# Optimization experiments

Measured on AMD Instinct MI355X. Metric: run time of the kernel, lower is better.

Reference implementation:

```python
import jax, jax.numpy as jnp
import numpy as np

NEG_SLOPE = 0.2

def setup_inputs() -> dict:
    key = jax.random.key(0)
    ks = jax.random.split(key, 6)
    N, C, H, E_DIM, E = 50000, 128, 64, 16, 800000
    x = jax.random.normal(ks[0], (N, C), dtype=jnp.float32)
    edge_index = jax.random.randint(ks[1], (2, E), 0, N, dtype=jnp.int64)
    edge_attr = jax.random.normal(ks[2], (E, E_DIM), dtype=jnp.float32)
    fc_w = jax.random.normal(ks[3], (H, C), dtype=jnp.float32) * (1.0 / np.sqrt(C))
    fc_b = jnp.zeros((H,), dtype=jnp.float32)
    att_w = jax.random.normal(ks[4], (H, 2 * H + E_DIM), dtype=jnp.float32) * (1.0 / np.sqrt(2 * H + E_DIM))
    att_b = jnp.zeros((H,), dtype=jnp.float32)
    return {"x": x, "edge_index": edge_index, "edge_attr": edge_attr,
            "fc_w": fc_w, "fc_b": fc_b, "att_w": att_w, "att_b": att_b}

def reference(x, edge_index, edge_attr, fc_w, fc_b, att_w, att_b):
    # Node projection: h = fc(x), [N, H]
    h = x @ fc_w.T + fc_b
    src = edge_index[0]  # i (destination of aggregation)
    dst = edge_index[1]  # j (neighbor whose features are aggregated)
    h_i = h[src]                      # [E, H]
    h_j = h[dst]                      # [E, H]
    feat = jnp.concatenate([h_i, h_j, edge_attr], axis=-1)  # [E, 2H+edge_dim]
    alpha = jax.nn.leaky_relu(feat @ att_w.T + att_b, negative_slope=NEG_SLOPE)  # [E, H]
    # dropout is identity in eval mode (training=False)
    msg = h_j * alpha                 # [E, H]
    out = jax.ops.segment_sum(msg, src, num_segments=h.shape[0])  # scatter-add into out[i]
    return out
```

## Files before the change

kernel.cpp:

```cpp
#include <hip/hip_runtime.h>


#define HID 64

__global__ __launch_bounds__(256) void node_kernel(
    const float* __restrict__ x,
    const float* __restrict__ fc_w, const float* __restrict__ fc_b,
    const float* __restrict__ att_w, const float* __restrict__ att_b,
    float* __restrict__ ai_out, float2* __restrict__ hjaj_out, int N)
{
    __shared__ __align__(16) float4 wF[64 * 32];
    __shared__ __align__(16) float4 wI[64 * 16];
    __shared__ __align__(16) float4 wJ[64 * 16];
    __shared__ __align__(16) float xs[4][128];
    __shared__ __align__(16) float hs[4][64];

    const int t = threadIdx.x;
    for (int idx = t; idx < 64 * 32; idx += 256) {
        int l = idx >> 5, c = idx & 31;
        wF[l * 32 + (c ^ (l & 31))] =
            *reinterpret_cast<const float4*>(fc_w + l * 128 + c * 4);
    }
    for (int idx = t; idx < 64 * 16; idx += 256) {
        int l = idx >> 4, c = idx & 15;
        wI[l * 16 + (c ^ (l & 15))] =
            *reinterpret_cast<const float4*>(att_w + l * 144 + c * 4);
        wJ[l * 16 + (c ^ (l & 15))] =
            *reinterpret_cast<const float4*>(att_w + l * 144 + 64 + c * 4);
    }
    __syncthreads();

    const int w = t >> 6, l = t & 63;
    const float bF = fc_b[l];
    const float bA = att_b[l];
    const int waveId = blockIdx.x * 4 + w;
    const int nWaves = gridDim.x * 4;

    for (int n = waveId; n < N; n += nWaves) {
        float2 xv = reinterpret_cast<const float2*>(x)[n * 64 + l];
        xs[w][2 * l] = xv.x;
        xs[w][2 * l + 1] = xv.y;
        float acc = bF;
        #pragma unroll
        for (int c = 0; c < 32; ++c) {
            float4 wv = wF[l * 32 + (c ^ (l & 31))];
            float4 xc = *reinterpret_cast<const float4*>(&xs[w][c * 4]);
            acc = fmaf(wv.x, xc.x, acc);
            acc = fmaf(wv.y, xc.y, acc);
            acc = fmaf(wv.z, xc.z, acc);
            acc = fmaf(wv.w, xc.w, acc);
        }
        hs[w][l] = acc;
        float a2 = bA, a3 = 0.f;
        #pragma unroll
        for (int c = 0; c < 16; ++c) {
            float4 hv = *reinterpret_cast<const float4*>(&hs[w][c * 4]);
            float4 wi = wI[l * 16 + (c ^ (l & 15))];
            float4 wj = wJ[l * 16 + (c ^ (l & 15))];
            a2 = fmaf(wi.x, hv.x, a2); a2 = fmaf(wi.y, hv.y, a2);
            a2 = fmaf(wi.z, hv.z, a2); a2 = fmaf(wi.w, hv.w, a2);
            a3 = fmaf(wj.x, hv.x, a3); a3 = fmaf(wj.y, hv.y, a3);
            a3 = fmaf(wj.z, hv.z, a3); a3 = fmaf(wj.w, hv.w, a3);
        }
        ai_out[n * 64 + l] = a2;
        hjaj_out[n * 64 + l] = make_float2(acc, a3);
    }
}

__global__ __launch_bounds__(256) void edge_kernel(
    const int* __restrict__ ei,
    const float* __restrict__ ea,
    const float* __restrict__ ai,
    const float2* __restrict__ hjaj,
    const float* __restrict__ att_w,
    float* __restrict__ out, int E)
{
    __shared__ __align__(16) float4 eas[4][256];

    const int t = threadIdx.x;
    const int w = t >> 6, l = t & 63;

    float we[16];
    #pragma unroll
    for (int k = 0; k < 16; ++k) we[k] = att_w[l * 144 + 128 + k];

    const int waveId = blockIdx.x * 4 + w;
    const int nWaves = gridDim.x * 4;
    const float4* ea4 = reinterpret_cast<const float4*>(ea);

    for (int e0 = waveId * 64; e0 < E; e0 += nWaves * 64) {
        const int nE = min(64, E - e0);
        int src = 0, dst = 0;
        if (l < nE) {
            src = ei[e0 + l];
            dst = ei[E + e0 + l];
        }
        #pragma unroll
        for (int r = 0; r < 4; ++r) {
            int f = r * 64 + l;
            if (f < nE * 4) eas[w][f] = ea4[(size_t)e0 * 4 + f];
        }
        asm volatile("s_waitcnt lgkmcnt(0)" ::: "memory");

        for (int e = 0; e < nE; ++e) {
            int s = __shfl(src, e);
            int d = __shfl(dst, e);
            float a_src = ai[s * 64 + l];
            float2 hd = hjaj[d * 64 + l];
            float4 v0 = eas[w][e * 4 + 0];
            float4 v1 = eas[w][e * 4 + 1];
            float4 v2 = eas[w][e * 4 + 2];
            float4 v3 = eas[w][e * 4 + 3];
            float pre = a_src + hd.y;
            pre = fmaf(we[0], v0.x, pre);  pre = fmaf(we[1], v0.y, pre);
            pre = fmaf(we[2], v0.z, pre);  pre = fmaf(we[3], v0.w, pre);
            pre = fmaf(we[4], v1.x, pre);  pre = fmaf(we[5], v1.y, pre);
            pre = fmaf(we[6], v1.z, pre);  pre = fmaf(we[7], v1.w, pre);
            pre = fmaf(we[8], v2.x, pre);  pre = fmaf(we[9], v2.y, pre);
            pre = fmaf(we[10], v2.z, pre); pre = fmaf(we[11], v2.w, pre);
            pre = fmaf(we[12], v3.x, pre); pre = fmaf(we[13], v3.y, pre);
            pre = fmaf(we[14], v3.z, pre); pre = fmaf(we[15], v3.w, pre);
            float alpha = pre > 0.f ? pre : 0.2f * pre;
            atomicAdd(&out[(size_t)s * 64 + l], hd.x * alpha);
        }
    }
}

extern "C" void kernel_launch(void* const* d_in, const int* in_sizes, int n_in,
                              void* d_out, int out_size, void* d_ws, size_t ws_size,
                              hipStream_t stream) {
    const float* x     = (const float*)d_in[0];
    const int*   ei    = (const int*)d_in[1];
    const float* ea    = (const float*)d_in[2];
    const float* fc_w  = (const float*)d_in[3];
    const float* fc_b  = (const float*)d_in[4];
    const float* att_w = (const float*)d_in[5];
    const float* att_b = (const float*)d_in[6];
    float* out = (float*)d_out;

    const int N = in_sizes[0] / 128;
    const int E = in_sizes[2] / 16;

    float*  ai   = (float*)d_ws;
    float2* hjaj = (float2*)((char*)d_ws + (size_t)N * 64 * sizeof(float));

    hipMemsetAsync(d_out, 0, (size_t)out_size * sizeof(float), stream);

    node_kernel<<<512, 256, 0, stream>>>(x, fc_w, fc_b, att_w, att_b, ai, hjaj, N);
    edge_kernel<<<1024, 256, 0, stream>>>(ei, ea, ai, hjaj, att_w, out, E);
}
```

Baseline: 284.0 us.

## Batch four edges per gather group and four nodes per wave in projection

Measured after the change: 266.8 us. 1.06x faster.

```diff
diff --git a/kernel.cpp b/kernel.cpp
--- a/kernel.cpp
+++ b/kernel.cpp
@@ -1,7 +1,5 @@
 #include <hip/hip_runtime.h>
 
-
-#define HID 64
 
 __global__ __launch_bounds__(256) void node_kernel(
     const float* __restrict__ x,
@@ -12,8 +10,8 @@
     __shared__ __align__(16) float4 wF[64 * 32];
     __shared__ __align__(16) float4 wI[64 * 16];
     __shared__ __align__(16) float4 wJ[64 * 16];
-    __shared__ __align__(16) float xs[4][128];
-    __shared__ __align__(16) float hs[4][64];
+    __shared__ __align__(16) float xs[4][4][128];
+    __shared__ __align__(16) float hs[4][4][64];
 
     const int t = threadIdx.x;
     for (int idx = t; idx < 64 * 32; idx += 256) {
@@ -35,35 +33,55 @@
     const float bA = att_b[l];
     const int waveId = blockIdx.x * 4 + w;
     const int nWaves = gridDim.x * 4;
-
-    for (int n = waveId; n < N; n += nWaves) {
-        float2 xv = reinterpret_cast<const float2*>(x)[n * 64 + l];
-        xs[w][2 * l] = xv.x;
-        xs[w][2 * l + 1] = xv.y;
-        float acc = bF;
+    const float2* x2 = reinterpret_cast<const float2*>(x);
+
+    for (int n0 = waveId * 4; n0 < N; n0 += nWaves * 4) {
+        const int nb = min(4, N - n0);
+        #pragma unroll
+        for (int m = 0; m < 4; ++m) {
+            if (m < nb) {
+                float2 xv = x2[(size_t)(n0 + m) * 64 + l];
+                xs[w][m][2 * l] = xv.x;
+                xs[w][m][2 * l + 1] = xv.y;
+            }
+        }
+        float acc[4] = {bF, bF, bF, bF};
         #pragma unroll
         for (int c = 0; c < 32; ++c) {
             float4 wv = wF[l * 32 + (c ^ (l & 31))];
-            float4 xc = *reinterpret_cast<const float4*>(&xs[w][c * 4]);
-            acc = fmaf(wv.x, xc.x, acc);
-            acc = fmaf(wv.y, xc.y, acc);
-            acc = fmaf(wv.z, xc.z, acc);
-            acc = fmaf(wv.w, xc.w, acc);
-        }
-        hs[w][l] = acc;
-        float a2 = bA, a3 = 0.f;
+            #pragma unroll
+            for (int m = 0; m < 4; ++m) {
+                float4 xc = *reinterpret_cast<const float4*>(&xs[w][m][c * 4]);
+                acc[m] = fmaf(wv.x, xc.x, acc[m]);
+                acc[m] = fmaf(wv.y, xc.y, acc[m]);
+                acc[m] = fmaf(wv.z, xc.z, acc[m]);
+                acc[m] = fmaf(wv.w, xc.w, acc[m]);
+            }
+        }
+        #pragma unroll
+        for (int m = 0; m < 4; ++m) hs[w][m][l] = acc[m];
+        float a2[4] = {bA, bA, bA, bA};
+        float a3[4] = {0.f, 0.f, 0.f, 0.f};
         #pragma unroll
         for (int c = 0; c < 16; ++c) {
-            float4 hv = *reinterpret_cast<const float4*>(&hs[w][c * 4]);
             float4 wi = wI[l * 16 + (c ^ (l & 15))];
             float4 wj = wJ[l * 16 + (c ^ (l & 15))];
-            a2 = fmaf(wi.x, hv.x, a2); a2 = fmaf(wi.y, hv.y, a2);
-            a2 = fmaf(wi.z, hv.z, a2); a2 = fmaf(wi.w, hv.w, a2);
-            a3 = fmaf(wj.x, hv.x, a3); a3 = fmaf(wj.y, hv.y, a3);
-            a3 = fmaf(wj.z, hv.z, a3); a3 = fmaf(wj.w, hv.w, a3);
-        }
-        ai_out[n * 64 + l] = a2;
-        hjaj_out[n * 64 + l] = make_float2(acc, a3);
+            #pragma unroll
+            for (int m = 0; m < 4; ++m) {
+                float4 hv = *reinterpret_cast<const float4*>(&hs[w][m][c * 4]);
+                a2[m] = fmaf(wi.x, hv.x, a2[m]); a2[m] = fmaf(wi.y, hv.y, a2[m]);
+                a2[m] = fmaf(wi.z, hv.z, a2[m]); a2[m] = fmaf(wi.w, hv.w, a2[m]);
+                a3[m] = fmaf(wj.x, hv.x, a3[m]); a3[m] = fmaf(wj.y, hv.y, a3[m]);
+                a3[m] = fmaf(wj.z, hv.z, a3[m]); a3[m] = fmaf(wj.w, hv.w, a3[m]);
+            }
+        }
+        #pragma unroll
+        for (int m = 0; m < 4; ++m) {
+            if (m < nb) {
+                ai_out[(size_t)(n0 + m) * 64 + l] = a2[m];
+                hjaj_out[(size_t)(n0 + m) * 64 + l] = make_float2(acc[m], a3[m]);
+            }
+        }
     }
 }
 
@@ -87,43 +105,75 @@
     const int waveId = blockIdx.x * 4 + w;
     const int nWaves = gridDim.x * 4;
     const float4* ea4 = reinterpret_cast<const float4*>(ea);
-
-    for (int e0 = waveId * 64; e0 < E; e0 += nWaves * 64) {
-        const int nE = min(64, E - e0);
+    const int fullE = E & ~63;
+
+#define EDGE_COMPUTE(S, HD, IDX)                                               \
+    {                                                                          \
+        float4 v0 = eas[w][(IDX) * 4 + 0];                                     \
+        float4 v1 = eas[w][(IDX) * 4 + 1];                                     \
+        float4 v2 = eas[w][(IDX) * 4 + 2];                                     \
+        float4 v3 = eas[w][(IDX) * 4 + 3];                                     \
+        float pre = (HD).y + a_##S;                                            \
+        pre = fmaf(we[0], v0.x, pre);  pre = fmaf(we[1], v0.y, pre);           \
+        pre = fmaf(we[2], v0.z, pre);  pre = fmaf(we[3], v0.w, pre);           \
+        pre = fmaf(we[4], v1.x, pre);  pre = fmaf(we[5], v1.y, pre);           \
+        pre = fmaf(we[6], v1.z, pre);  pre = fmaf(we[7], v1.w, pre);           \
+        pre = fmaf(we[8], v2.x, pre);  pre = fmaf(we[9], v2.y, pre);           \
+        pre = fmaf(we[10], v2.z, pre); pre = fmaf(we[11], v2.w, pre);          \
+        pre = fmaf(we[12], v3.x, pre); pre = fmaf(we[13], v3.y, pre);          \
+        pre = fmaf(we[14], v3.z, pre); pre = fmaf(we[15], v3.w, pre);          \
+        float alpha = pre > 0.f ? pre : 0.2f * pre;                            \
+        atomicAdd(&out[(size_t)s_##S * 64 + l], (HD).x * alpha);               \
+    }
+
+    for (int e0 = waveId * 64; e0 < fullE; e0 += nWaves * 64) {
+        int src = ei[e0 + l];
+        int dst = ei[E + e0 + l];
+        #pragma unroll
+        for (int r = 0; r < 4; ++r)
+            eas[w][r * 64 + l] = ea4[(size_t)e0 * 4 + r * 64 + l];
+        asm volatile("s_waitcnt lgkmcnt(0)" ::: "memory");
+
+        #pragma unroll 1
+        for (int g = 0; g < 64; g += 4) {
+            int s_0 = __shfl(src, g + 0), s_1 = __shfl(src, g + 1);
+            int s_2 = __shfl(src, g + 2), s_3 = __shfl(src, g + 3);
+            int d_0 = __shfl(dst, g + 0), d_1 = __shfl(dst, g + 1);
+            int d_2 = __shfl(dst, g + 2), d_3 = __shfl(dst, g + 3);
+            float a_0 = ai[(size_t)s_0 * 64 + l];
+            float a_1 = ai[(size_t)s_1 * 64 + l];
+            float a_2 = ai[(size_t)s_2 * 64 + l];
+            float a_3 = ai[(size_t)s_3 * 64 + l];
+            float2 h0 = hjaj[(size_t)d_0 * 64 + l];
+            float2 h1 = hjaj[(size_t)d_1 * 64 + l];
+            float2 h2 = hjaj[(size_t)d_2 * 64 + l];
+            float2 h3 = hjaj[(size_t)d_3 * 64 + l];
+            EDGE_COMPUTE(0, h0, g + 0);
+            EDGE_COMPUTE(1, h1, g + 1);
+            EDGE_COMPUTE(2, h2, g + 2);
+            EDGE_COMPUTE(3, h3, g + 3);
+        }
+    }
+
+    if (E > fullE && waveId == 0) {
+        const int nE = E - fullE;
         int src = 0, dst = 0;
-        if (l < nE) {
-            src = ei[e0 + l];
-            dst = ei[E + e0 + l];
-        }
+        if (l < nE) { src = ei[fullE + l]; dst = ei[E + fullE + l]; }
         #pragma unroll
         for (int r = 0; r < 4; ++r) {
             int f = r * 64 + l;
-            if (f < nE * 4) eas[w][f] = ea4[(size_t)e0 * 4 + f];
+            if (f < nE * 4) eas[w][f] = ea4[(size_t)fullE * 4 + f];
         }
         asm volatile("s_waitcnt lgkmcnt(0)" ::: "memory");
-
         for (int e = 0; e < nE; ++e) {
-            int s = __shfl(src, e);
-            int d = __shfl(dst, e);
-            float a_src = ai[s * 64 + l];
-            float2 hd = hjaj[d * 64 + l];
-            float4 v0 = eas[w][e * 4 + 0];
-            float4 v1 = eas[w][e * 4 + 1];
-            float4 v2 = eas[w][e * 4 + 2];
-            float4 v3 = eas[w][e * 4 + 3];
-            float pre = a_src + hd.y;
-            pre = fmaf(we[0], v0.x, pre);  pre = fmaf(we[1], v0.y, pre);
-            pre = fmaf(we[2], v0.z, pre);  pre = fmaf(we[3], v0.w, pre);
-            pre = fmaf(we[4], v1.x, pre);  pre = fmaf(we[5], v1.y, pre);
-            pre = fmaf(we[6], v1.z, pre);  pre = fmaf(we[7], v1.w, pre);
-            pre = fmaf(we[8], v2.x, pre);  pre = fmaf(we[9], v2.y, pre);
-            pre = fmaf(we[10], v2.z, pre); pre = fmaf(we[11], v2.w, pre);
-            pre = fmaf(we[12], v3.x, pre); pre = fmaf(we[13], v3.y, pre);
-            pre = fmaf(we[14], v3.z, pre); pre = fmaf(we[15], v3.w, pre);
-            float alpha = pre > 0.f ? pre : 0.2f * pre;
-            atomicAdd(&out[(size_t)s * 64 + l], hd.x * alpha);
-        }
-    }
+            int s_0 = __shfl(src, e);
+            int d_0 = __shfl(dst, e);
+            float a_0 = ai[(size_t)s_0 * 64 + l];
+            float2 h0 = hjaj[(size_t)d_0 * 64 + l];
+            EDGE_COMPUTE(0, h0, e);
+        }
+    }
+#undef EDGE_COMPUTE
 }
 
 extern "C" void kernel_launch(void* const* d_in, const int* in_sizes, int n_in,
@@ -147,5 +197,5 @@
     hipMemsetAsync(d_out, 0, (size_t)out_size * sizeof(float), stream);
 
     node_kernel<<<512, 256, 0, stream>>>(x, fc_w, fc_b, att_w, att_b, ai, hjaj, N);
-    edge_kernel<<<1024, 256, 0, stream>>>(ei, ea, ai, hjaj, att_w, out, E);
+    edge_kernel<<<2048, 256, 0, stream>>>(ei, ea, ai, hjaj, att_w, out, E);
 }
```

## Software-pipeline edge gathers, one tile per wave, and batch two nodes per wave

Applied to the files above, without the earlier changes.

After: 450.9 us. 58.8% more time.

```diff
diff --git a/kernel.cpp b/kernel.cpp
--- a/kernel.cpp
+++ b/kernel.cpp
@@ -1,9 +1,7 @@
 #include <hip/hip_runtime.h>
 
 
-#define HID 64
-
-__global__ __launch_bounds__(256) void node_kernel(
+__global__ __launch_bounds__(512) void node_kernel(
     const float* __restrict__ x,
     const float* __restrict__ fc_w, const float* __restrict__ fc_b,
     const float* __restrict__ att_w, const float* __restrict__ att_b,
@@ -12,16 +10,16 @@
     __shared__ __align__(16) float4 wF[64 * 32];
     __shared__ __align__(16) float4 wI[64 * 16];
     __shared__ __align__(16) float4 wJ[64 * 16];
-    __shared__ __align__(16) float xs[4][128];
-    __shared__ __align__(16) float hs[4][64];
+    __shared__ __align__(16) float xs[8][2][128];
+    __shared__ __align__(16) float hs[8][2][64];
 
     const int t = threadIdx.x;
-    for (int idx = t; idx < 64 * 32; idx += 256) {
+    for (int idx = t; idx < 64 * 32; idx += 512) {
         int l = idx >> 5, c = idx & 31;
         wF[l * 32 + (c ^ (l & 31))] =
             *reinterpret_cast<const float4*>(fc_w + l * 128 + c * 4);
     }
-    for (int idx = t; idx < 64 * 16; idx += 256) {
+    for (int idx = t; idx < 64 * 16; idx += 512) {
         int l = idx >> 4, c = idx & 15;
         wI[l * 16 + (c ^ (l & 15))] =
             *reinterpret_cast<const float4*>(att_w + l * 144 + c * 4);
@@ -33,37 +31,57 @@
     const int w = t >> 6, l = t & 63;
     const float bF = fc_b[l];
     const float bA = att_b[l];
-    const int waveId = blockIdx.x * 4 + w;
-    const int nWaves = gridDim.x * 4;
-
-    for (int n = waveId; n < N; n += nWaves) {
-        float2 xv = reinterpret_cast<const float2*>(x)[n * 64 + l];
-        xs[w][2 * l] = xv.x;
-        xs[w][2 * l + 1] = xv.y;
-        float acc = bF;
+    const int waveId = blockIdx.x * 8 + w;
+    const int nWaves = gridDim.x * 8;
+    const float2* x2 = reinterpret_cast<const float2*>(x);
+
+    for (int n0 = waveId * 2; n0 < N; n0 += nWaves * 2) {
+        const int nb = min(2, N - n0);
+        #pragma unroll
+        for (int m = 0; m < 2; ++m) {
+            if (m < nb) {
+                float2 xv = x2[(size_t)(n0 + m) * 64 + l];
+                xs[w][m][2 * l] = xv.x;
+                xs[w][m][2 * l + 1] = xv.y;
+            }
+        }
+        float acc[2] = {bF, bF};
         #pragma unroll
         for (int c = 0; c < 32; ++c) {
             float4 wv = wF[l * 32 + (c ^ (l & 31))];
-            float4 xc = *reinterpret_cast<const float4*>(&xs[w][c * 4]);
-            acc = fmaf(wv.x, xc.x, acc);
-            acc = fmaf(wv.y, xc.y, acc);
-            acc = fmaf(wv.z, xc.z, acc);
-            acc = fmaf(wv.w, xc.w, acc);
-        }
-        hs[w][l] = acc;
-        float a2 = bA, a3 = 0.f;
+            #pragma unroll
+            for (int m = 0; m < 2; ++m) {
+                float4 xc = *reinterpret_cast<const float4*>(&xs[w][m][c * 4]);
+                acc[m] = fmaf(wv.x, xc.x, acc[m]);
+                acc[m] = fmaf(wv.y, xc.y, acc[m]);
+                acc[m] = fmaf(wv.z, xc.z, acc[m]);
+                acc[m] = fmaf(wv.w, xc.w, acc[m]);
+            }
+        }
+        #pragma unroll
+        for (int m = 0; m < 2; ++m) hs[w][m][l] = acc[m];
+        float a2[2] = {bA, bA};
+        float a3[2] = {0.f, 0.f};
         #pragma unroll
         for (int c = 0; c < 16; ++c) {
-            float4 hv = *reinterpret_cast<const float4*>(&hs[w][c * 4]);
             float4 wi = wI[l * 16 + (c ^ (l & 15))];
             float4 wj = wJ[l * 16 + (c ^ (l & 15))];
-            a2 = fmaf(wi.x, hv.x, a2); a2 = fmaf(wi.y, hv.y, a2);
-            a2 = fmaf(wi.z, hv.z, a2); a2 = fmaf(wi.w, hv.w, a2);
-            a3 = fmaf(wj.x, hv.x, a3); a3 = fmaf(wj.y, hv.y, a3);
-            a3 = fmaf(wj.z, hv.z, a3); a3 = fmaf(wj.w, hv.w, a3);
-        }
-        ai_out[n * 64 + l] = a2;
-        hjaj_out[n * 64 + l] = make_float2(acc, a3);
+            #pragma unroll
+            for (int m = 0; m < 2; ++m) {
+                float4 hv = *reinterpret_cast<const float4*>(&hs[w][m][c * 4]);
+                a2[m] = fmaf(wi.x, hv.x, a2[m]); a2[m] = fmaf(wi.y, hv.y, a2[m]);
+                a2[m] = fmaf(wi.z, hv.z, a2[m]); a2[m] = fmaf(wi.w, hv.w, a2[m]);
+                a3[m] = fmaf(wj.x, hv.x, a3[m]); a3[m] = fmaf(wj.y, hv.y, a3[m]);
+                a3[m] = fmaf(wj.z, hv.z, a3[m]); a3[m] = fmaf(wj.w, hv.w, a3[m]);
+            }
+        }
+        #pragma unroll
+        for (int m = 0; m < 2; ++m) {
+            if (m < nb) {
+                ai_out[(size_t)(n0 + m) * 64 + l] = a2[m];
+                hjaj_out[(size_t)(n0 + m) * 64 + l] = make_float2(acc[m], a3[m]);
+            }
+        }
     }
 }
 
@@ -85,33 +103,77 @@
     for (int k = 0; k < 16; ++k) we[k] = att_w[l * 144 + 128 + k];
 
     const int waveId = blockIdx.x * 4 + w;
-    const int nWaves = gridDim.x * 4;
+    const int e0 = waveId * 64;
+    if (e0 >= E) return;
+    const int nE = min(64, E - e0);
+
+    int src = 0, dst = 0;
+    if (l < nE) { src = ei[e0 + l]; dst = ei[E + e0 + l]; }
     const float4* ea4 = reinterpret_cast<const float4*>(ea);
-
-    for (int e0 = waveId * 64; e0 < E; e0 += nWaves * 64) {
-        const int nE = min(64, E - e0);
-        int src = 0, dst = 0;
-        if (l < nE) {
-            src = ei[e0 + l];
-            dst = ei[E + e0 + l];
-        }
-        #pragma unroll
-        for (int r = 0; r < 4; ++r) {
-            int f = r * 64 + l;
-            if (f < nE * 4) eas[w][f] = ea4[(size_t)e0 * 4 + f];
-        }
-        asm volatile("s_waitcnt lgkmcnt(0)" ::: "memory");
-
+    #pragma unroll
+    for (int r = 0; r < 4; ++r) {
+        int f = r * 64 + l;
+        if (f < nE * 4) eas[w][f] = ea4[(size_t)e0 * 4 + f];
+    }
+    asm volatile("s_waitcnt lgkmcnt(0)" ::: "memory");
+
+#define LOADG(S, g)                                                            \
+    {                                                                          \
+        _Pragma("unroll") for (int e = 0; e < 4; ++e) {                        \
+            s##S[e] = __shfl(src, (g) * 4 + e);                                \
+            int dd = __shfl(dst, (g) * 4 + e);                                 \
+            a##S[e] = ai[(size_t)s##S[e] * 64 + l];                            \
+            h##S[e] = hjaj[(size_t)dd * 64 + l];                               \
+        }                                                                      \
+    }
+
+#define COMPG(S, g)                                                            \
+    {                                                                          \
+        _Pragma("unroll") for (int e = 0; e < 4; ++e) {                        \
+            float4 v0 = eas[w][((g) * 4 + e) * 4 + 0];                         \
+            float4 v1 = eas[w][((g) * 4 + e) * 4 + 1];                         \
+            float4 v2 = eas[w][((g) * 4 + e) * 4 + 2];                         \
+            float4 v3 = eas[w][((g) * 4 + e) * 4 + 3];                         \
+            float pre = h##S[e].y + a##S[e];                                   \
+            pre = fmaf(we[0], v0.x, pre);  pre = fmaf(we[1], v0.y, pre);       \
+            pre = fmaf(we[2], v0.z, pre);  pre = fmaf(we[3], v0.w, pre);       \
+            pre = fmaf(we[4], v1.x, pre);  pre = fmaf(we[5], v1.y, pre);       \
+            pre = fmaf(we[6], v1.z, pre);  pre = fmaf(we[7], v1.w, pre);       \
+            pre = fmaf(we[8], v2.x, pre);  pre = fmaf(we[9], v2.y, pre);       \
+            pre = fmaf(we[10], v2.z, pre); pre = fmaf(we[11], v2.w, pre);      \
+            pre = fmaf(we[12], v3.x, pre); pre = fmaf(we[13], v3.y, pre);      \
+            pre = fmaf(we[14], v3.z, pre); pre = fmaf(we[15], v3.w, pre);      \
+            float alpha = pre > 0.f ? pre : 0.2f * pre;                        \
+            atomicAdd(&out[(size_t)s##S[e] * 64 + l], h##S[e].x * alpha);      \
+        }                                                                      \
+    }
+
+    if (nE == 64) {
+        int sA[4], sB[4];
+        float aA[4], aB[4];
+        float2 hA[4], hB[4];
+        LOADG(A, 0);
+        #pragma unroll
+        for (int g = 0; g < 16; g += 2) {
+            if (g + 1 < 16) LOADG(B, g + 1);
+            COMPG(A, g);
+            if (g + 2 < 16) LOADG(A, g + 2);
+            COMPG(B, g + 1);
+        }
+    } else {
+        int sA[1];
+        float aA[1];
+        float2 hA[1];
         for (int e = 0; e < nE; ++e) {
-            int s = __shfl(src, e);
-            int d = __shfl(dst, e);
-            float a_src = ai[s * 64 + l];
-            float2 hd = hjaj[d * 64 + l];
+            sA[0] = __shfl(src, e);
+            int dd = __shfl(dst, e);
+            aA[0] = ai[(size_t)sA[0] * 64 + l];
+            hA[0] = hjaj[(size_t)dd * 64 + l];
             float4 v0 = eas[w][e * 4 + 0];
             float4 v1 = eas[w][e * 4 + 1];
             float4 v2 = eas[w][e * 4 + 2];
             float4 v3 = eas[w][e * 4 + 3];
-            float pre = a_src + hd.y;
+            float pre = hA[0].y + aA[0];
             pre = fmaf(we[0], v0.x, pre);  pre = fmaf(we[1], v0.y, pre);
             pre = fmaf(we[2], v0.z, pre);  pre = fmaf(we[3], v0.w, pre);
             pre = fmaf(we[4], v1.x, pre);  pre = fmaf(we[5], v1.y, pre);
@@ -121,9 +183,11 @@
             pre = fmaf(we[12], v3.x, pre); pre = fmaf(we[13], v3.y, pre);
             pre = fmaf(we[14], v3.z, pre); pre = fmaf(we[15], v3.w, pre);
             float alpha = pre > 0.f ? pre : 0.2f * pre;
-            atomicAdd(&out[(size_t)s * 64 + l], hd.x * alpha);
-        }
-    }
+            atomicAdd(&out[(size_t)sA[0] * 64 + l], hA[0].x * alpha);
+        }
+    }
+#undef LOADG
+#undef COMPG
 }
 
 extern "C" void kernel_launch(void* const* d_in, const int* in_sizes, int n_in,
@@ -146,6 +210,9 @@
 
     hipMemsetAsync(d_out, 0, (size_t)out_size * sizeof(float), stream);
 
-    node_kernel<<<512, 256, 0, stream>>>(x, fc_w, fc_b, att_w, att_b, ai, hjaj, N);
-    edge_kernel<<<1024, 256, 0, stream>>>(ei, ea, ai, hjaj, att_w, out, E);
+    node_kernel<<<512, 512, 0, stream>>>(x, fc_w, fc_b, att_w, att_b, ai, hjaj, N);
+
+    const int tiles = (E + 63) / 64;
+    const int eblocks = (tiles + 3) / 4;
+    edge_kernel<<<eblocks, 256, 0, stream>>>(ei, ea, ai, hjaj, att_w, out, E);
 }
```

## Replace atomic edge scatter with per-launch CSR build and per-node gather

Applied to the files above, without the earlier changes.

Result: slower. 324.8 us (+14.4%).

```diff
diff --git a/kernel.cpp b/kernel.cpp
--- a/kernel.cpp
+++ b/kernel.cpp
@@ -1,13 +1,12 @@
 #include <hip/hip_runtime.h>
 
-
-#define HID 64
 
 __global__ __launch_bounds__(256) void node_kernel(
     const float* __restrict__ x,
     const float* __restrict__ fc_w, const float* __restrict__ fc_b,
     const float* __restrict__ att_w, const float* __restrict__ att_b,
-    float* __restrict__ ai_out, float2* __restrict__ hjaj_out, int N)
+    float* __restrict__ ai_out, float* __restrict__ h_out,
+    float* __restrict__ aj_out, int N)
 {
     __shared__ __align__(16) float4 wF[64 * 32];
     __shared__ __align__(16) float4 wI[64 * 16];
@@ -37,7 +36,7 @@
     const int nWaves = gridDim.x * 4;
 
     for (int n = waveId; n < N; n += nWaves) {
-        float2 xv = reinterpret_cast<const float2*>(x)[n * 64 + l];
+        float2 xv = reinterpret_cast<const float2*>(x)[(size_t)n * 64 + l];
         xs[w][2 * l] = xv.x;
         xs[w][2 * l + 1] = xv.y;
         float acc = bF;
@@ -54,76 +53,172 @@
         float a2 = bA, a3 = 0.f;
         #pragma unroll
         for (int c = 0; c < 16; ++c) {
-            float4 hv = *reinterpret_cast<const float4*>(&hs[w][c * 4]);
+            float4 hvv = *reinterpret_cast<const float4*>(&hs[w][c * 4]);
             float4 wi = wI[l * 16 + (c ^ (l & 15))];
             float4 wj = wJ[l * 16 + (c ^ (l & 15))];
-            a2 = fmaf(wi.x, hv.x, a2); a2 = fmaf(wi.y, hv.y, a2);
-            a2 = fmaf(wi.z, hv.z, a2); a2 = fmaf(wi.w, hv.w, a2);
-            a3 = fmaf(wj.x, hv.x, a3); a3 = fmaf(wj.y, hv.y, a3);
-            a3 = fmaf(wj.z, hv.z, a3); a3 = fmaf(wj.w, hv.w, a3);
-        }
-        ai_out[n * 64 + l] = a2;
-        hjaj_out[n * 64 + l] = make_float2(acc, a3);
-    }
-}
-
-__global__ __launch_bounds__(256) void edge_kernel(
-    const int* __restrict__ ei,
-    const float* __restrict__ ea,
-    const float* __restrict__ ai,
-    const float2* __restrict__ hjaj,
-    const float* __restrict__ att_w,
-    float* __restrict__ out, int E)
-{
-    __shared__ __align__(16) float4 eas[4][256];
-
-    const int t = threadIdx.x;
-    const int w = t >> 6, l = t & 63;
+            a2 = fmaf(wi.x, hvv.x, a2); a2 = fmaf(wi.y, hvv.y, a2);
+            a2 = fmaf(wi.z, hvv.z, a2); a2 = fmaf(wi.w, hvv.w, a2);
+            a3 = fmaf(wj.x, hvv.x, a3); a3 = fmaf(wj.y, hvv.y, a3);
+            a3 = fmaf(wj.z, hvv.z, a3); a3 = fmaf(wj.w, hvv.w, a3);
+        }
+        ai_out[(size_t)n * 64 + l] = a2;
+        h_out[(size_t)n * 64 + l]  = acc;
+        aj_out[(size_t)n * 64 + l] = a3;
+    }
+}
+
+__global__ __launch_bounds__(256) void hist_kernel(
+    const int* __restrict__ ei, int* __restrict__ count, int E)
+{
+    int i = blockIdx.x * 256 + threadIdx.x;
+    int stride = gridDim.x * 256;
+    for (; i < E; i += stride) atomicAdd(&count[ei[i]], 1);
+}
+
+__global__ __launch_bounds__(256) void scan1_kernel(
+    const int* __restrict__ count, int* __restrict__ start,
+    int* __restrict__ bsum, int N)
+{
+    __shared__ int wsum[4];
+    const int t = threadIdx.x, blk = blockIdx.x;
+    const int idx0 = blk * 1024 + t * 4;
+    int c0 = 0, c1 = 0, c2 = 0, c3 = 0;
+    if (idx0 + 3 < N) {
+        int4 c = *reinterpret_cast<const int4*>(count + idx0);
+        c0 = c.x; c1 = c.y; c2 = c.z; c3 = c.w;
+    } else {
+        if (idx0 + 0 < N) c0 = count[idx0 + 0];
+        if (idx0 + 1 < N) c1 = count[idx0 + 1];
+        if (idx0 + 2 < N) c2 = count[idx0 + 2];
+    }
+    const int s = c0 + c1 + c2 + c3;
+    const int lane = t & 63, w = t >> 6;
+    int v = s;
+    #pragma unroll
+    for (int off = 1; off < 64; off <<= 1) {
+        int u = __shfl_up(v, off);
+        if (lane >= off) v += u;
+    }
+    if (lane == 63) wsum[w] = v;
+    __syncthreads();
+    int base = 0;
+    if (w > 0) base += wsum[0];
+    if (w > 1) base += wsum[1];
+    if (w > 2) base += wsum[2];
+    const int excl = base + v - s;
+    if (idx0 + 0 < N) start[idx0 + 0] = excl;
+    if (idx0 + 1 < N) start[idx0 + 1] = excl + c0;
+    if (idx0 + 2 < N) start[idx0 + 2] = excl + c0 + c1;
+    if (idx0 + 3 < N) start[idx0 + 3] = excl + c0 + c1 + c2;
+    if (t == 255) bsum[blk] = base + v;
+}
+
+__global__ void scan2_kernel(int* __restrict__ bsum, int nb)
+{
+    const int l = threadIdx.x;
+    int v = (l < nb) ? bsum[l] : 0;
+    int inc = v;
+    #pragma unroll
+    for (int off = 1; off < 64; off <<= 1) {
+        int u = __shfl_up(inc, off);
+        if (l >= off) inc += u;
+    }
+    if (l < nb) bsum[l] = inc - v;
+}
+
+__global__ __launch_bounds__(256) void scan3_kernel(
+    int* __restrict__ start, const int* __restrict__ bsum, int N)
+{
+    const int blk = blockIdx.x;
+    const int add = bsum[blk];
+    #pragma unroll
+    for (int q = 0; q < 4; ++q) {
+        int i = blk * 1024 + q * 256 + threadIdx.x;
+        if (i < N) start[i] += add;
+    }
+}
+
+__global__ __launch_bounds__(256) void scatter_kernel(
+    const int* __restrict__ ei, const int* __restrict__ start,
+    int* __restrict__ cursor, int2* __restrict__ sd, int E)
+{
+    int i = blockIdx.x * 256 + threadIdx.x;
+    int stride = gridDim.x * 256;
+    for (; i < E; i += stride) {
+        int s = ei[i];
+        int pos = start[s] + atomicAdd(&cursor[s], 1);
+        sd[pos] = make_int2(ei[E + i], i);
+    }
+}
+
+__global__ __launch_bounds__(256) void csr_edge_kernel(
+    const int2* __restrict__ sd, const int* __restrict__ start,
+    const int* __restrict__ count,
+    const float* __restrict__ ai, const float* __restrict__ hv,
+    const float* __restrict__ aj, const float* __restrict__ ea,
+    const float* __restrict__ att_w, float* __restrict__ out, int N)
+{
+    const int t = threadIdx.x, w = t >> 6, l = t & 63;
+    const int n = blockIdx.x * 4 + w;
+    if (n >= N) return;
 
     float we[16];
     #pragma unroll
     for (int k = 0; k < 16; ++k) we[k] = att_w[l * 144 + 128 + k];
 
-    const int waveId = blockIdx.x * 4 + w;
-    const int nWaves = gridDim.x * 4;
-    const float4* ea4 = reinterpret_cast<const float4*>(ea);
-
-    for (int e0 = waveId * 64; e0 < E; e0 += nWaves * 64) {
-        const int nE = min(64, E - e0);
-        int src = 0, dst = 0;
-        if (l < nE) {
-            src = ei[e0 + l];
-            dst = ei[E + e0 + l];
-        }
-        #pragma unroll
-        for (int r = 0; r < 4; ++r) {
-            int f = r * 64 + l;
-            if (f < nE * 4) eas[w][f] = ea4[(size_t)e0 * 4 + f];
-        }
-        asm volatile("s_waitcnt lgkmcnt(0)" ::: "memory");
-
-        for (int e = 0; e < nE; ++e) {
-            int s = __shfl(src, e);
-            int d = __shfl(dst, e);
-            float a_src = ai[s * 64 + l];
-            float2 hd = hjaj[d * 64 + l];
-            float4 v0 = eas[w][e * 4 + 0];
-            float4 v1 = eas[w][e * 4 + 1];
-            float4 v2 = eas[w][e * 4 + 2];
-            float4 v3 = eas[w][e * 4 + 3];
-            float pre = a_src + hd.y;
-            pre = fmaf(we[0], v0.x, pre);  pre = fmaf(we[1], v0.y, pre);
-            pre = fmaf(we[2], v0.z, pre);  pre = fmaf(we[3], v0.w, pre);
-            pre = fmaf(we[4], v1.x, pre);  pre = fmaf(we[5], v1.y, pre);
-            pre = fmaf(we[6], v1.z, pre);  pre = fmaf(we[7], v1.w, pre);
-            pre = fmaf(we[8], v2.x, pre);  pre = fmaf(we[9], v2.y, pre);
-            pre = fmaf(we[10], v2.z, pre); pre = fmaf(we[11], v2.w, pre);
-            pre = fmaf(we[12], v3.x, pre); pre = fmaf(we[13], v3.y, pre);
-            pre = fmaf(we[14], v3.z, pre); pre = fmaf(we[15], v3.w, pre);
-            float alpha = pre > 0.f ? pre : 0.2f * pre;
-            atomicAdd(&out[(size_t)s * 64 + l], hd.x * alpha);
-        }
-    }
+    const int deg = count[n];
+    const int base = start[n];
+    const float aiv = ai[(size_t)n * 64 + l];
+    float acc = 0.f;
+
+#define EDOT(pre, id)                                                          \
+    {                                                                          \
+        const float4* er = reinterpret_cast<const float4*>(ea + (size_t)(id) * 16); \
+        float4 v0 = er[0], v1 = er[1], v2 = er[2], v3 = er[3];                 \
+        pre = fmaf(we[0], v0.x, pre);  pre = fmaf(we[1], v0.y, pre);           \
+        pre = fmaf(we[2], v0.z, pre);  pre = fmaf(we[3], v0.w, pre);           \
+        pre = fmaf(we[4], v1.x, pre);  pre = fmaf(we[5], v1.y, pre);           \
+        pre = fmaf(we[6], v1.z, pre);  pre = fmaf(we[7], v1.w, pre);           \
+        pre = fmaf(we[8], v2.x, pre);  pre = fmaf(we[9], v2.y, pre);           \
+        pre = fmaf(we[10], v2.z, pre); pre = fmaf(we[11], v2.w, pre);          \
+        pre = fmaf(we[12], v3.x, pre); pre = fmaf(we[13], v3.y, pre);          \
+        pre = fmaf(we[14], v3.z, pre); pre = fmaf(we[15], v3.w, pre);          \
+    }
+
+    int done = 0;
+    while (done < deg) {
+        const int rem = min(64, deg - done);
+        int2 v = make_int2(0, 0);
+        if (l < rem) v = sd[base + done + l];
+        int k = 0;
+        for (; k + 4 <= rem; k += 4) {
+            int d0 = __shfl(v.x, k + 0), i0 = __shfl(v.y, k + 0);
+            int d1 = __shfl(v.x, k + 1), i1 = __shfl(v.y, k + 1);
+            int d2 = __shfl(v.x, k + 2), i2 = __shfl(v.y, k + 2);
+            int d3 = __shfl(v.x, k + 3), i3 = __shfl(v.y, k + 3);
+            float h0 = hv[(size_t)d0 * 64 + l], j0 = aj[(size_t)d0 * 64 + l];
+            float h1 = hv[(size_t)d1 * 64 + l], j1 = aj[(size_t)d1 * 64 + l];
+            float h2 = hv[(size_t)d2 * 64 + l], j2 = aj[(size_t)d2 * 64 + l];
+            float h3 = hv[(size_t)d3 * 64 + l], j3 = aj[(size_t)d3 * 64 + l];
+            float p0 = aiv + j0; EDOT(p0, i0);
+            float a0 = p0 > 0.f ? p0 : 0.2f * p0; acc = fmaf(h0, a0, acc);
+            float p1 = aiv + j1; EDOT(p1, i1);
+            float a1 = p1 > 0.f ? p1 : 0.2f * p1; acc = fmaf(h1, a1, acc);
+            float p2 = aiv + j2; EDOT(p2, i2);
+            float a2 = p2 > 0.f ? p2 : 0.2f * p2; acc = fmaf(h2, a2, acc);
+            float p3 = aiv + j3; EDOT(p3, i3);
+            float a3 = p3 > 0.f ? p3 : 0.2f * p3; acc = fmaf(h3, a3, acc);
+        }
+        for (; k < rem; ++k) {
+            int d0 = __shfl(v.x, k), i0 = __shfl(v.y, k);
+            float h0 = hv[(size_t)d0 * 64 + l], j0 = aj[(size_t)d0 * 64 + l];
+            float p0 = aiv + j0; EDOT(p0, i0);
+            float a0 = p0 > 0.f ? p0 : 0.2f * p0; acc = fmaf(h0, a0, acc);
+        }
+        done += rem;
+    }
+#undef EDOT
+    out[(size_t)n * 64 + l] = acc;
 }
 
 extern "C" void kernel_launch(void* const* d_in, const int* in_sizes, int n_in,
@@ -141,11 +236,30 @@
     const int N = in_sizes[0] / 128;
     const int E = in_sizes[2] / 16;
 
-    float*  ai   = (float*)d_ws;
-    float2* hjaj = (float2*)((char*)d_ws + (size_t)N * 64 * sizeof(float));
-
-    hipMemsetAsync(d_out, 0, (size_t)out_size * sizeof(float), stream);
-
-    node_kernel<<<512, 256, 0, stream>>>(x, fc_w, fc_b, att_w, att_b, ai, hjaj, N);
-    edge_kernel<<<1024, 256, 0, stream>>>(ei, ea, ai, hjaj, att_w, out, E);
-}
+    char* wsb = (char*)d_ws;
+    float* ai    = (float*)wsb;
+    float* hvp   = ai + (size_t)N * 64;
+    float* ajp   = hvp + (size_t)N * 64;
+    int* count   = (int*)(ajp + (size_t)N * 64);
+    int* cursor  = count + N;
+    int* startp  = cursor + N;
+    int* bsum    = startp + N;
+    size_t sd_off = (((size_t)(bsum + 64) - (size_t)wsb) + 255) & ~(size_t)255;
+    int2* sd     = (int2*)(wsb + sd_off);
+
+    hipMemsetAsync(count, 0, 2 * (size_t)N * sizeof(int), stream);
+
+    node_kernel<<<512, 256, 0, stream>>>(x, fc_w, fc_b, att_w, att_b, ai, hvp, ajp, N);
+
+    hist_kernel<<<1024, 256, 0, stream>>>(ei, count, E);
+
+    const int nb1 = (N + 1023) / 1024;
+    scan1_kernel<<<nb1, 256, 0, stream>>>(count, startp, bsum, N);
+    scan2_kernel<<<1, 64, 0, stream>>>(bsum, nb1);
+    scan3_kernel<<<nb1, 256, 0, stream>>>(startp, bsum, N);
+
+    scatter_kernel<<<1024, 256, 0, stream>>>(ei, startp, cursor, sd, E);
+
+    csr_edge_kernel<<<(N + 3) / 4, 256, 0, stream>>>(
+        sd, startp, count, ai, hvp, ajp, ea, att_w, out, N);
+}
```
